# Kernel tuning notes

Hardware: AMD Instinct MI355X
Metric: run time of the kernel (lower is better)

## Reference

```python
import jax, jax.numpy as jnp
import numpy as np

N_NODES = 100000
N_EDGES = 1600000
IN_DIM = 128
OUT_DIM = 128
LEAKY_SLOPE = 0.01  # torch nn.LeakyReLU default


def setup_inputs() -> dict:
    key = jax.random.key(0)
    k1, k2, k3, k4 = jax.random.split(key, 4)
    x = jax.random.normal(k1, (N_NODES, IN_DIM), dtype=jnp.float32)
    edge_index = jax.random.randint(k2, (2, N_EDGES), 0, N_NODES, dtype=jnp.int64)
    edge_attr = jax.random.uniform(k3, (N_EDGES,), dtype=jnp.float32)
    # Linear params (xavier_uniform weight, zero bias)
    limit = np.sqrt(6.0 / (IN_DIM + OUT_DIM)).astype(np.float32)
    W = jax.random.uniform(k4, (OUT_DIM, IN_DIM), minval=-limit, maxval=limit, dtype=jnp.float32)
    b = jnp.zeros((OUT_DIM,), dtype=jnp.float32)
    return {"x": x, "edge_index": edge_index, "edge_attr": edge_attr, "W": W, "b": b}


def reference(x, edge_index, edge_attr, W, b):
    src = edge_index[0]  # x_j (source nodes)
    dst = edge_index[1]  # aggregation index (target nodes)
    # message: gather source features, scale by per-edge scalar  [E, D]
    msg = x[src] * edge_attr[:, None]
    # aggregate: scatter-add over target index  [N, D]
    agg = jax.ops.segment_sum(msg, dst, num_segments=N_NODES)
    # update: Linear + LeakyReLU (dropout is identity at p=0 / eval)
    out = agg @ W.T + b
    return jnp.where(out >= 0, out, LEAKY_SLOPE * out)
```

## Files before the change

kernel.cpp:

```cpp
#include <hip/hip_runtime.h>

#define N_NODES 100000
#define N_EDGES 1600000
#define DIM 128
#define LEAKY 0.01f
#define RS_STRIDE 132
#define WS_STRIDE 132
#define LSTRIDE 132
#define NBUCKET 391
#define SB_EDGES 4096
#define NSB 391

typedef short bf16x8 __attribute__((ext_vector_type(8)));
typedef float f32x4 __attribute__((ext_vector_type(4)));

static __device__ __forceinline__ unsigned short f2bf(float f) {
  unsigned int u = __float_as_uint(f);
  u = (u + 0x7fffu + ((u >> 16) & 1u)) >> 16;
  return (unsigned short)u;
}

__global__ __launch_bounds__(512) void sort_local_kernel(
    const int* __restrict__ ei, const float* __restrict__ attr,
    int2* __restrict__ binned, unsigned short* __restrict__ counts,
    int* __restrict__ srcOff) {
  __shared__ int hist[NBUCKET];
  __shared__ int cursor[NBUCKET];
  __shared__ int scanBuf[512];
  __shared__ int2 stage[SB_EDGES];

  const int t = threadIdx.x;
  const int blk = blockIdx.x;
  const int base = blk * SB_EDGES;
  const int n = min(SB_EDGES, N_EDGES - base);

  if (t < NBUCKET) hist[t] = 0;
  __syncthreads();

  int myP[8];
  int myB[8];
  float myA[8];
#pragma unroll
  for (int k = 0; k < 8; ++k) {
    int i = t + k * 512;
    if (i < n) {
      int e = base + i;
      int s = ei[e];
      int d = ei[N_EDGES + e];
      myA[k] = attr[e];
      myB[k] = d >> 8;
      myP[k] = s | ((d & 255) << 17);
      atomicAdd(&hist[myB[k]], 1);
    } else {
      myB[k] = -1;
    }
  }
  __syncthreads();

  int v = (t < NBUCKET) ? hist[t] : 0;
  scanBuf[t] = v;
  __syncthreads();
  for (int off = 1; off < 512; off <<= 1) {
    int u = (t >= off) ? scanBuf[t - off] : 0;
    __syncthreads();
    scanBuf[t] += u;
    __syncthreads();
  }
  if (t < NBUCKET) {
    int excl = scanBuf[t] - v;
    cursor[t] = excl;
    counts[(size_t)t * NSB + blk] = (unsigned short)v;
    srcOff[(size_t)t * NSB + blk] = base + excl;
  }
  __syncthreads();

#pragma unroll
  for (int k = 0; k < 8; ++k) {
    if (myB[k] >= 0) {
      int loc = atomicAdd(&cursor[myB[k]], 1);
      stage[loc] = make_int2(myP[k], __float_as_int(myA[k]));
    }
  }
  __syncthreads();

  for (int i = t; i < n; i += 512) binned[base + i] = stage[i];
}

__global__ __launch_bounds__(128) void bucket_count_kernel(
    const unsigned short* __restrict__ counts, int* __restrict__ bucketCount) {
  __shared__ int red[128];
  const int b = blockIdx.x;
  const int t = threadIdx.x;
  int s = 0;
  for (int sb = t; sb < NSB; sb += 128) s += counts[(size_t)b * NSB + sb];
  red[t] = s;
  __syncthreads();
  for (int off = 64; off > 0; off >>= 1) {
    if (t < off) red[t] += red[t + off];
    __syncthreads();
  }
  if (t == 0) bucketCount[b] = red[0];
}

__global__ __launch_bounds__(512) void bucket_scan_kernel(
    const int* __restrict__ bucketCount, int* __restrict__ bucketBase) {
  __shared__ int s[512];
  const int t = threadIdx.x;
  int v = (t < NBUCKET) ? bucketCount[t] : 0;
  s[t] = v;
  __syncthreads();
  for (int off = 1; off < 512; off <<= 1) {
    int u = (t >= off) ? s[t - off] : 0;
    __syncthreads();
    s[t] += u;
    __syncthreads();
  }
  if (t < NBUCKET) bucketBase[t] = s[t] - v;
}

__global__ __launch_bounds__(448) void passB_kernel(
    const int2* __restrict__ binned, const unsigned short* __restrict__ counts,
    const int* __restrict__ srcOff, const int* __restrict__ bucketBase,
    int2* __restrict__ csr, int* __restrict__ row_ptr) {
  __shared__ int runSrc[NSB];
  __shared__ int runLen[NSB];
  __shared__ int hist[256];
  __shared__ int cur[256];
  __shared__ int scanBuf[256];

  const int b = blockIdx.x;
  const int t = threadIdx.x;

  if (t < NSB) {
    runSrc[t] = srcOff[(size_t)b * NSB + t];
    runLen[t] = (int)counts[(size_t)b * NSB + t];
  }
  if (t < 256) hist[t] = 0;
  __syncthreads();

  if (t < NSB) {
    const int src = runSrc[t];
    const int len = runLen[t];
    for (int j = 0; j < len; ++j) {
      int px = binned[src + j].x;
      atomicAdd(&hist[(px >> 17) & 255], 1);
    }
  }
  __syncthreads();

  int hv = (t < 256) ? hist[t] : 0;
  if (t < 256) scanBuf[t] = hv;
  __syncthreads();
  for (int off = 1; off < 256; off <<= 1) {
    int u = 0;
    if (t < 256 && t >= off) u = scanBuf[t - off];
    __syncthreads();
    if (t < 256) scanBuf[t] += u;
    __syncthreads();
  }
  const int bb = bucketBase[b];
  if (t < 256) {
    int excl = scanBuf[t] - hv;
    cur[t] = excl;
    int node = b * 256 + t;
    if (node < N_NODES) row_ptr[node] = bb + excl;
  }
  if (b == 0 && t == 0) row_ptr[N_NODES] = N_EDGES;
  __syncthreads();

  if (t < NSB) {
    const int src = runSrc[t];
    const int len = runLen[t];
    for (int j = 0; j < len; ++j) {
      int2 rec = binned[src + j];
      int ld = (rec.x >> 17) & 255;
      int pos = bb + atomicAdd(&cur[ld], 1);
      csr[pos] = make_int2(rec.x & 0x1FFFF, rec.y);
    }
  }
}

__global__ __launch_bounds__(256) void x2b_kernel(
    const float4* __restrict__ x, ushort4* __restrict__ xb) {
  const int i = blockIdx.x * 256 + threadIdx.x;
  float4 v = x[i];
  ushort4 o;
  o.x = f2bf(v.x); o.y = f2bf(v.y); o.z = f2bf(v.z); o.w = f2bf(v.w);
  xb[i] = o;
}

__global__ __launch_bounds__(256) void gather_linear_kernel(
    const unsigned short* __restrict__ xb, const int* __restrict__ row_ptr,
    const int2* __restrict__ csr, const bf16x8* __restrict__ wfrag,
    const float* __restrict__ bias, float* __restrict__ out) {
  __shared__ float Ls[16 * LSTRIDE];

  const int w = threadIdx.x >> 6;
  const int lane = threadIdx.x & 63;
  const int nodeBase = blockIdx.x * 16;

#pragma unroll
  for (int k = 0; k < 4; ++k) {
    const int loc = w * 4 + k;
    const int node = nodeBase + loc;
    const int beg = row_ptr[node];
    const int end = row_ptr[node + 1];

    float2 acc = make_float2(0.f, 0.f);
    int e = beg;
    for (; e + 3 < end; e += 4) {
      int2 e0 = csr[e];
      int2 e1 = csr[e + 1];
      int2 e2 = csr[e + 2];
      int2 e3 = csr[e + 3];
      unsigned int u0 = *(const unsigned int*)(xb + (size_t)e0.x * DIM + lane * 2);
      unsigned int u1 = *(const unsigned int*)(xb + (size_t)e1.x * DIM + lane * 2);
      unsigned int u2 = *(const unsigned int*)(xb + (size_t)e2.x * DIM + lane * 2);
      unsigned int u3 = *(const unsigned int*)(xb + (size_t)e3.x * DIM + lane * 2);
      float a0 = __int_as_float(e0.y), a1 = __int_as_float(e1.y);
      float a2 = __int_as_float(e2.y), a3 = __int_as_float(e3.y);
      acc.x += __uint_as_float(u0 << 16) * a0;
      acc.y += __uint_as_float(u0 & 0xffff0000u) * a0;
      acc.x += __uint_as_float(u1 << 16) * a1;
      acc.y += __uint_as_float(u1 & 0xffff0000u) * a1;
      acc.x += __uint_as_float(u2 << 16) * a2;
      acc.y += __uint_as_float(u2 & 0xffff0000u) * a2;
      acc.x += __uint_as_float(u3 << 16) * a3;
      acc.y += __uint_as_float(u3 & 0xffff0000u) * a3;
    }
    for (; e < end; ++e) {
      int2 e0 = csr[e];
      float a0 = __int_as_float(e0.y);
      unsigned int u0 = *(const unsigned int*)(xb + (size_t)e0.x * DIM + lane * 2);
      acc.x += __uint_as_float(u0 << 16) * a0;
      acc.y += __uint_as_float(u0 & 0xffff0000u) * a0;
    }
    *(float2*)(Ls + loc * LSTRIDE + lane * 2) = acc;
  }
  __syncthreads();

  const int m = lane & 15;
  const int quad = lane >> 4;

  bf16x8 afrag[4];
#pragma unroll
  for (int q = 0; q < 4; ++q) {
    const float* ap = Ls + m * LSTRIDE + q * 32 + quad * 8;
    const float4 f0 = *(const float4*)(ap);
    const float4 f1 = *(const float4*)(ap + 4);
    afrag[q][0] = (short)f2bf(f0.x); afrag[q][1] = (short)f2bf(f0.y);
    afrag[q][2] = (short)f2bf(f0.z); afrag[q][3] = (short)f2bf(f0.w);
    afrag[q][4] = (short)f2bf(f1.x); afrag[q][5] = (short)f2bf(f1.y);
    afrag[q][6] = (short)f2bf(f1.z); afrag[q][7] = (short)f2bf(f1.w);
  }

#pragma unroll
  for (int j = 0; j < 2; ++j) {
    const int nt = w * 2 + j;
    const float bv = bias[nt * 16 + m];
    f32x4 acc = {bv, bv, bv, bv};
#pragma unroll
    for (int q = 0; q < 4; ++q) {
      bf16x8 bfrag = wfrag[(nt * 4 + q) * 64 + lane];
      acc = __builtin_amdgcn_mfma_f32_16x16x32_bf16(afrag[q], bfrag, acc, 0, 0, 0);
    }
    const int col = nt * 16 + m;
#pragma unroll
    for (int i = 0; i < 4; ++i) {
      float v = acc[i];
      v = v >= 0.f ? v : v * LEAKY;
      out[(size_t)(nodeBase + quad * 4 + i) * DIM + col] = v;
    }
  }
}

__global__ __launch_bounds__(256) void gather_f32_kernel(
    const float* __restrict__ x, const int* __restrict__ row_ptr,
    const int2* __restrict__ csr, float* __restrict__ out) {
  const int node = blockIdx.x * 4 + (threadIdx.x >> 6);
  const int lane = threadIdx.x & 63;

  const int beg = row_ptr[node];
  const int end = row_ptr[node + 1];

  float2 acc = make_float2(0.f, 0.f);
  int e = beg;
  for (; e + 3 < end; e += 4) {
    int2 e0 = csr[e];
    int2 e1 = csr[e + 1];
    int2 e2 = csr[e + 2];
    int2 e3 = csr[e + 3];
    float2 v0 = *(const float2*)(x + (size_t)e0.x * DIM + lane * 2);
    float2 v1 = *(const float2*)(x + (size_t)e1.x * DIM + lane * 2);
    float2 v2 = *(const float2*)(x + (size_t)e2.x * DIM + lane * 2);
    float2 v3 = *(const float2*)(x + (size_t)e3.x * DIM + lane * 2);
    float a0 = __int_as_float(e0.y), a1 = __int_as_float(e1.y);
    float a2 = __int_as_float(e2.y), a3 = __int_as_float(e3.y);
    acc.x += v0.x * a0; acc.y += v0.y * a0;
    acc.x += v1.x * a1; acc.y += v1.y * a1;
    acc.x += v2.x * a2; acc.y += v2.y * a2;
    acc.x += v3.x * a3; acc.y += v3.y * a3;
  }
  for (; e < end; ++e) {
    int2 e0 = csr[e];
    float a0 = __int_as_float(e0.y);
    float2 v0 = *(const float2*)(x + (size_t)e0.x * DIM + lane * 2);
    acc.x += v0.x * a0; acc.y += v0.y * a0;
  }
  *(float2*)(out + (size_t)node * DIM + lane * 2) = acc;
}

__global__ __launch_bounds__(256) void w_frag_kernel(
    const float* __restrict__ W, bf16x8* __restrict__ wfrag) {
  const int gid = blockIdx.x * 256 + threadIdx.x;
  const int lane = gid & 63;
  const int q = (gid >> 6) & 3;
  const int nt = gid >> 8;
  const int n = nt * 16 + (lane & 15);
  const int kb = q * 32 + ((lane >> 4) & 3) * 8;
  const float4 f0 = *(const float4*)(W + n * DIM + kb);
  const float4 f1 = *(const float4*)(W + n * DIM + kb + 4);
  bf16x8 frag;
  frag[0] = (short)f2bf(f0.x); frag[1] = (short)f2bf(f0.y);
  frag[2] = (short)f2bf(f0.z); frag[3] = (short)f2bf(f0.w);
  frag[4] = (short)f2bf(f1.x); frag[5] = (short)f2bf(f1.y);
  frag[6] = (short)f2bf(f1.z); frag[7] = (short)f2bf(f1.w);
  wfrag[gid] = frag;
}

__global__ __launch_bounds__(256) void linear_mfma_kernel(
    const float* __restrict__ agg, const bf16x8* __restrict__ wfrag,
    const float* __restrict__ bias, float* __restrict__ out) {
  const int wave = threadIdx.x >> 6;
  const int lane = threadIdx.x & 63;
  const int r0 = (blockIdx.x * 4 + wave) * 16;
  if (r0 >= N_NODES) return;

  const int m = lane & 15;
  const int quad = lane >> 4;
  const int row = r0 + m;

  bf16x8 afrag[4];
#pragma unroll
  for (int q = 0; q < 4; ++q) {
    const float* ap = agg + (size_t)row * DIM + q * 32 + quad * 8;
    const float4 f0 = *(const float4*)(ap);
    const float4 f1 = *(const float4*)(ap + 4);
    afrag[q][0] = (short)f2bf(f0.x); afrag[q][1] = (short)f2bf(f0.y);
    afrag[q][2] = (short)f2bf(f0.z); afrag[q][3] = (short)f2bf(f0.w);
    afrag[q][4] = (short)f2bf(f1.x); afrag[q][5] = (short)f2bf(f1.y);
    afrag[q][6] = (short)f2bf(f1.z); afrag[q][7] = (short)f2bf(f1.w);
  }

#pragma unroll
  for (int nt = 0; nt < 8; ++nt) {
    const float bv = bias[nt * 16 + m];
    f32x4 acc = {bv, bv, bv, bv};
#pragma unroll
    for (int q = 0; q < 4; ++q) {
      bf16x8 bfrag = wfrag[(nt * 4 + q) * 64 + lane];
      acc = __builtin_amdgcn_mfma_f32_16x16x32_bf16(afrag[q], bfrag, acc, 0, 0, 0);
    }
    const int col = nt * 16 + m;
#pragma unroll
    for (int i = 0; i < 4; ++i) {
      float v = acc[i];
      v = v >= 0.f ? v : v * LEAKY;
      out[(size_t)(r0 + quad * 4 + i) * DIM + col] = v;
    }
  }
}

__global__ __launch_bounds__(256) void scatter_kernel(
    const float* __restrict__ x, const int* __restrict__ ei,
    const float* __restrict__ attr, float* __restrict__ agg) {
  int gid = blockIdx.x * blockDim.x + threadIdx.x;
  int e = gid >> 5;
  int f = (gid & 31) * 4;
  if (e >= N_EDGES) return;
  int s = ei[e];
  int d = ei[N_EDGES + e];
  float a = attr[e];
  const float4 xv = *(const float4*)(x + (size_t)s * DIM + f);
  float* dp = agg + (size_t)d * DIM + f;
  atomicAdd(dp + 0, xv.x * a);
  atomicAdd(dp + 1, xv.y * a);
  atomicAdd(dp + 2, xv.z * a);
  atomicAdd(dp + 3, xv.w * a);
}

__global__ __launch_bounds__(256, 2) void linear_kernel(
    const float* __restrict__ agg, const float* __restrict__ W,
    const float* __restrict__ bias, float* __restrict__ out) {
  __shared__ float Rs[32 * RS_STRIDE];
  __shared__ float Ws[64 * WS_STRIDE];

  const int tid = threadIdx.x;
  const int c = (tid & 31) * 4;
  const int rg = tid >> 5;
  const size_t rowBase = (size_t)blockIdx.x * 32;

  {
    const int lr = tid >> 3;
    const int col = (tid & 7) * 16;
    const float4* src = (const float4*)(agg + (rowBase + lr) * DIM + col);
#pragma unroll
    for (int j = 0; j < 4; ++j) {
      *(float4*)(Rs + lr * RS_STRIDE + col + j * 4) = src[j];
    }
  }

  const float4 bv = *(const float4*)(bias + c);
  float4 acc0 = bv, acc1 = bv, acc2 = bv, acc3 = bv;

  for (int half = 0; half < 2; ++half) {
    __syncthreads();
    {
      const int k0 = tid >> 7;
      const int o = tid & 127;
#pragma unroll
      for (int kk = k0; kk < 64; kk += 2) {
        Ws[kk * WS_STRIDE + o] = W[o * DIM + half * 64 + kk];
      }
    }
    __syncthreads();

    const float* rs0 = Rs + (rg * 4 + 0) * RS_STRIDE + half * 64;
    const float* rs1 = Rs + (rg * 4 + 1) * RS_STRIDE + half * 64;
    const float* rs2 = Rs + (rg * 4 + 2) * RS_STRIDE + half * 64;
    const float* rs3 = Rs + (rg * 4 + 3) * RS_STRIDE + half * 64;

#pragma unroll 8
    for (int k4 = 0; k4 < 16; ++k4) {
      const float4 v0 = *(const float4*)(rs0 + k4 * 4);
      const float4 v1 = *(const float4*)(rs1 + k4 * 4);
      const float4 v2 = *(const float4*)(rs2 + k4 * 4);
      const float4 v3 = *(const float4*)(rs3 + k4 * 4);
      const float4 w0 = *(const float4*)(Ws + (k4 * 4 + 0) * WS_STRIDE + c);
      const float4 w1 = *(const float4*)(Ws + (k4 * 4 + 1) * WS_STRIDE + c);
      const float4 w2 = *(const float4*)(Ws + (k4 * 4 + 2) * WS_STRIDE + c);
      const float4 w3 = *(const float4*)(Ws + (k4 * 4 + 3) * WS_STRIDE + c);

#define FMA4(acc, v)                                               \
      acc.x += v.x * w0.x + v.y * w1.x + v.z * w2.x + v.w * w3.x;  \
      acc.y += v.x * w0.y + v.y * w1.y + v.z * w2.y + v.w * w3.y;  \
      acc.z += v.x * w0.z + v.y * w1.z + v.z * w2.z + v.w * w3.z;  \
      acc.w += v.x * w0.w + v.y * w1.w + v.z * w2.w + v.w * w3.w;
      FMA4(acc0, v0)
      FMA4(acc1, v1)
      FMA4(acc2, v2)
      FMA4(acc3, v3)
#undef FMA4
    }
  }

#define LEAKY4(acc)                                   \
  acc.x = acc.x >= 0.f ? acc.x : acc.x * LEAKY;       \
  acc.y = acc.y >= 0.f ? acc.y : acc.y * LEAKY;       \
  acc.z = acc.z >= 0.f ? acc.z : acc.z * LEAKY;       \
  acc.w = acc.w >= 0.f ? acc.w : acc.w * LEAKY;
  LEAKY4(acc0) LEAKY4(acc1) LEAKY4(acc2) LEAKY4(acc3)
#undef LEAKY4

  const int row0 = (int)rowBase + rg * 4;
  *(float4*)(out + (size_t)(row0 + 0) * DIM + c) = acc0;
  *(float4*)(out + (size_t)(row0 + 1) * DIM + c) = acc1;
  *(float4*)(out + (size_t)(row0 + 2) * DIM + c) = acc2;
  *(float4*)(out + (size_t)(row0 + 3) * DIM + c) = acc3;
}

extern "C" void kernel_launch(void* const* d_in, const int* in_sizes, int n_in,
                              void* d_out, int out_size, void* d_ws, size_t ws_size,
                              hipStream_t stream) {
  const float* x = (const float*)d_in[0];
  const int* ei = (const int*)d_in[1];
  const float* attr = (const float*)d_in[2];
  const float* W = (const float*)d_in[3];
  const float* b = (const float*)d_in[4];
  float* out = (float*)d_out;

  const size_t offBinned = 0;
  const size_t offCounts = 12812288;
  const size_t offSrcOff = offCounts + 305920;
  const size_t offBCount = offSrcOff + 611584;
  const size_t offBBase  = offBCount + 1792;
  const size_t offCsr    = offBBase + 1792;
  const size_t offRowPtr = offCsr + 12812288;
  const size_t offWfrag  = offRowPtr + 400128;
  const size_t sortNeed  = offWfrag + 32768;
  const size_t offXb     = sortNeed;
  const size_t fullNeed  = offXb + 25600000;

  if (ws_size >= sortNeed) {
    char* ws = (char*)d_ws;
    int2* binned = (int2*)(ws + offBinned);
    unsigned short* counts = (unsigned short*)(ws + offCounts);
    int* srcOff = (int*)(ws + offSrcOff);
    int* bucketCount = (int*)(ws + offBCount);
    int* bucketBase = (int*)(ws + offBBase);
    int2* csr = (int2*)(ws + offCsr);
    int* row_ptr = (int*)(ws + offRowPtr);
    bf16x8* wfrag = (bf16x8*)(ws + offWfrag);

    w_frag_kernel<<<8, 256, 0, stream>>>(W, wfrag);
    sort_local_kernel<<<NSB, 512, 0, stream>>>(ei, attr, binned, counts, srcOff);
    bucket_count_kernel<<<NBUCKET, 128, 0, stream>>>(counts, bucketCount);
    bucket_scan_kernel<<<1, 512, 0, stream>>>(bucketCount, bucketBase);
    passB_kernel<<<NBUCKET, 448, 0, stream>>>(binned, counts, srcOff, bucketBase,
                                              csr, row_ptr);
    if (ws_size >= fullNeed) {
      unsigned short* xb = (unsigned short*)(ws + offXb);
      x2b_kernel<<<12500, 256, 0, stream>>>((const float4*)x, (ushort4*)xb);
      gather_linear_kernel<<<N_NODES / 16, 256, 0, stream>>>(xb, row_ptr, csr,
                                                             wfrag, b, out);
    } else {
      gather_f32_kernel<<<N_NODES / 4, 256, 0, stream>>>(x, row_ptr, csr, out);
      linear_mfma_kernel<<<(N_NODES + 63) / 64, 256, 0, stream>>>(out, wfrag, b, out);
    }
  } else {
    hipMemsetAsync(out, 0, (size_t)N_NODES * DIM * sizeof(float), stream);
    scatter_kernel<<<(N_EDGES * 32) / 256, 256, 0, stream>>>(x, ei, attr, out);
    linear_kernel<<<N_NODES / 32, 256, 0, stream>>>(out, W, b, out);
  }
}
```

Measured before the change: 261.9 us.

## Split gather and linear, fuse x-to-bf16 conversion into sort kernel

Folds the fp32-to-bf16 conversion of x into the tail of the sort_local kernel, so the separate conversion launch disappears and the conversion runs alongside the sort. Replaces the fused gather+linear kernel with a one-node-per-wave gather that writes a bf16 aggregate buffer, followed by a separate MFMA linear kernel that loads bf16 fragments directly. This drops the LDS staging and barrier from the gather and raises its occupancy, at the cost of an extra 25.6 MB round trip through global memory for the aggregate and one more launch. It also needs more workspace, and falls back to the older paths when the workspace is too small.

```diff
diff --git a/kernel.cpp b/kernel.cpp
--- a/kernel.cpp
+++ b/kernel.cpp
@@ -6,7 +6,6 @@
 #define LEAKY 0.01f
 #define RS_STRIDE 132
 #define WS_STRIDE 132
-#define LSTRIDE 132
 #define NBUCKET 391
 #define SB_EDGES 4096
 #define NSB 391
@@ -23,7 +22,8 @@
 __global__ __launch_bounds__(512) void sort_local_kernel(
     const int* __restrict__ ei, const float* __restrict__ attr,
     int2* __restrict__ binned, unsigned short* __restrict__ counts,
-    int* __restrict__ srcOff) {
+    int* __restrict__ srcOff, const float4* __restrict__ x4,
+    ushort4* __restrict__ xb4) {
   __shared__ int hist[NBUCKET];
   __shared__ int cursor[NBUCKET];
   __shared__ int scanBuf[512];
@@ -84,6 +84,15 @@
   __syncthreads();
 
   for (int i = t; i < n; i += 512) binned[base + i] = stage[i];
+
+  if (xb4) {
+    for (int i = blk * 512 + t; i < (N_NODES * DIM) / 4; i += NSB * 512) {
+      float4 vv = x4[i];
+      ushort4 o;
+      o.x = f2bf(vv.x); o.y = f2bf(vv.y); o.z = f2bf(vv.z); o.w = f2bf(vv.w);
+      xb4[i] = o;
+    }
+  }
 }
 
 __global__ __launch_bounds__(128) void bucket_count_kernel(
@@ -180,98 +189,87 @@
   }
 }
 
-__global__ __launch_bounds__(256) void x2b_kernel(
-    const float4* __restrict__ x, ushort4* __restrict__ xb) {
-  const int i = blockIdx.x * 256 + threadIdx.x;
-  float4 v = x[i];
-  ushort4 o;
-  o.x = f2bf(v.x); o.y = f2bf(v.y); o.z = f2bf(v.z); o.w = f2bf(v.w);
-  xb[i] = o;
-}
-
-__global__ __launch_bounds__(256) void gather_linear_kernel(
+__global__ __launch_bounds__(256) void gather_aggb_kernel(
     const unsigned short* __restrict__ xb, const int* __restrict__ row_ptr,
-    const int2* __restrict__ csr, const bf16x8* __restrict__ wfrag,
-    const float* __restrict__ bias, float* __restrict__ out) {
-  __shared__ float Ls[16 * LSTRIDE];
-
-  const int w = threadIdx.x >> 6;
+    const int2* __restrict__ csr, unsigned int* __restrict__ aggB) {
+  const int node = blockIdx.x * 4 + (threadIdx.x >> 6);
   const int lane = threadIdx.x & 63;
-  const int nodeBase = blockIdx.x * 16;
-
-#pragma unroll
-  for (int k = 0; k < 4; ++k) {
-    const int loc = w * 4 + k;
-    const int node = nodeBase + loc;
-    const int beg = row_ptr[node];
-    const int end = row_ptr[node + 1];
-
-    float2 acc = make_float2(0.f, 0.f);
-    int e = beg;
-    for (; e + 3 < end; e += 4) {
-      int2 e0 = csr[e];
-      int2 e1 = csr[e + 1];
-      int2 e2 = csr[e + 2];
-      int2 e3 = csr[e + 3];
-      unsigned int u0 = *(const unsigned int*)(xb + (size_t)e0.x * DIM + lane * 2);
-      unsigned int u1 = *(const unsigned int*)(xb + (size_t)e1.x * DIM + lane * 2);
-      unsigned int u2 = *(const unsigned int*)(xb + (size_t)e2.x * DIM + lane * 2);
-      unsigned int u3 = *(const unsigned int*)(xb + (size_t)e3.x * DIM + lane * 2);
-      float a0 = __int_as_float(e0.y), a1 = __int_as_float(e1.y);
-      float a2 = __int_as_float(e2.y), a3 = __int_as_float(e3.y);
-      acc.x += __uint_as_float(u0 << 16) * a0;
-      acc.y += __uint_as_float(u0 & 0xffff0000u) * a0;
-      acc.x += __uint_as_float(u1 << 16) * a1;
-      acc.y += __uint_as_float(u1 & 0xffff0000u) * a1;
-      acc.x += __uint_as_float(u2 << 16) * a2;
-      acc.y += __uint_as_float(u2 & 0xffff0000u) * a2;
-      acc.x += __uint_as_float(u3 << 16) * a3;
-      acc.y += __uint_as_float(u3 & 0xffff0000u) * a3;
-    }
-    for (; e < end; ++e) {
-      int2 e0 = csr[e];
-      float a0 = __int_as_float(e0.y);
-      unsigned int u0 = *(const unsigned int*)(xb + (size_t)e0.x * DIM + lane * 2);
-      acc.x += __uint_as_float(u0 << 16) * a0;
-      acc.y += __uint_as_float(u0 & 0xffff0000u) * a0;
-    }
-    *(float2*)(Ls + loc * LSTRIDE + lane * 2) = acc;
-  }
-  __syncthreads();
-
-  const int m = lane & 15;
-  const int quad = lane >> 4;
-
-  bf16x8 afrag[4];
-#pragma unroll
-  for (int q = 0; q < 4; ++q) {
-    const float* ap = Ls + m * LSTRIDE + q * 32 + quad * 8;
-    const float4 f0 = *(const float4*)(ap);
-    const float4 f1 = *(const float4*)(ap + 4);
-    afrag[q][0] = (short)f2bf(f0.x); afrag[q][1] = (short)f2bf(f0.y);
-    afrag[q][2] = (short)f2bf(f0.z); afrag[q][3] = (short)f2bf(f0.w);
-    afrag[q][4] = (short)f2bf(f1.x); afrag[q][5] = (short)f2bf(f1.y);
-    afrag[q][6] = (short)f2bf(f1.z); afrag[q][7] = (short)f2bf(f1.w);
-  }
-
-#pragma unroll
-  for (int j = 0; j < 2; ++j) {
-    const int nt = w * 2 + j;
-    const float bv = bias[nt * 16 + m];
-    f32x4 acc = {bv, bv, bv, bv};
-#pragma unroll
-    for (int q = 0; q < 4; ++q) {
-      bf16x8 bfrag = wfrag[(nt * 4 + q) * 64 + lane];
-      acc = __builtin_amdgcn_mfma_f32_16x16x32_bf16(afrag[q], bfrag, acc, 0, 0, 0);
-    }
-    const int col = nt * 16 + m;
-#pragma unroll
-    for (int i = 0; i < 4; ++i) {
-      float v = acc[i];
-      v = v >= 0.f ? v : v * LEAKY;
-      out[(size_t)(nodeBase + quad * 4 + i) * DIM + col] = v;
-    }
-  }
+
+  const int beg = row_ptr[node];
+  const int end = row_ptr[node + 1];
+
+  float2 acc = make_float2(0.f, 0.f);
+  int e = beg;
+  for (; e + 3 < end; e += 4) {
+    int2 e0 = csr[e];
+    int2 e1 = csr[e + 1];
+    int2 e2 = csr[e + 2];
+    int2 e3 = csr[e + 3];
+    unsigned int u0 = *(const unsigned int*)(xb + (size_t)e0.x * DIM + lane * 2);
+    unsigned int u1 = *(const unsigned int*)(xb + (size_t)e1.x * DIM + lane * 2);
+    unsigned int u2 = *(const unsigned int*)(xb + (size_t)e2.x * DIM + lane * 2);
+    unsigned int u3 = *(const unsigned int*)(xb + (size_t)e3.x * DIM + lane * 2);
+    float a0 = __int_as_float(e0.y), a1 = __int_as_float(e1.y);
+    float a2 = __int_as_float(e2.y), a3 = __int_as_float(e3.y);
+    acc.x += __uint_as_float(u0 << 16) * a0;
+    acc.y += __uint_as_float(u0 & 0xffff0000u) * a0;
+    acc.x += __uint_as_float(u1 << 16) * a1;
+    acc.y += __uint_as_float(u1 & 0xffff0000u) * a1;
+    acc.x += __uint_as_float(u2 << 16) * a2;
+    acc.y += __uint_as_float(u2 & 0xffff0000u) * a2;
+    acc.x += __uint_as_float(u3 << 16) * a3;
+    acc.y += __uint_as_float(u3 & 0xffff0000u) * a3;
+  }
+  for (; e < end; ++e) {
+    int2 e0 = csr[e];
+    float a0 = __int_as_float(e0.y);
+    unsigned int u0 = *(const unsigned int*)(xb + (size_t)e0.x * DIM + lane * 2);
+    acc.x += __uint_as_float(u0 << 16) * a0;
+    acc.y += __uint_as_float(u0 & 0xffff0000u) * a0;
+  }
+  aggB[(size_t)node * 64 + lane] =
+      (unsigned int)f2bf(acc.x) | ((unsigned int)f2bf(acc.y) << 16);
+}
+
+__global__ __launch_bounds__(256) void gather_bf16_kernel(
+    const unsigned short* __restrict__ xb, const int* __restrict__ row_ptr,
+    const int2* __restrict__ csr, float* __restrict__ out) {
+  const int node = blockIdx.x * 4 + (threadIdx.x >> 6);
+  const int lane = threadIdx.x & 63;
+
+  const int beg = row_ptr[node];
+  const int end = row_ptr[node + 1];
+
+  float2 acc = make_float2(0.f, 0.f);
+  int e = beg;
+  for (; e + 3 < end; e += 4) {
+    int2 e0 = csr[e];
+    int2 e1 = csr[e + 1];
+    int2 e2 = csr[e + 2];
+    int2 e3 = csr[e + 3];
+    unsigned int u0 = *(const unsigned int*)(xb + (size_t)e0.x * DIM + lane * 2);
+    unsigned int u1 = *(const unsigned int*)(xb + (size_t)e1.x * DIM + lane * 2);
+    unsigned int u2 = *(const unsigned int*)(xb + (size_t)e2.x * DIM + lane * 2);
+    unsigned int u3 = *(const unsigned int*)(xb + (size_t)e3.x * DIM + lane * 2);
+    float a0 = __int_as_float(e0.y), a1 = __int_as_float(e1.y);
+    float a2 = __int_as_float(e2.y), a3 = __int_as_float(e3.y);
+    acc.x += __uint_as_float(u0 << 16) * a0;
+    acc.y += __uint_as_float(u0 & 0xffff0000u) * a0;
+    acc.x += __uint_as_float(u1 << 16) * a1;
+    acc.y += __uint_as_float(u1 & 0xffff0000u) * a1;
+    acc.x += __uint_as_float(u2 << 16) * a2;
+    acc.y += __uint_as_float(u2 & 0xffff0000u) * a2;
+    acc.x += __uint_as_float(u3 << 16) * a3;
+    acc.y += __uint_as_float(u3 & 0xffff0000u) * a3;
+  }
+  for (; e < end; ++e) {
+    int2 e0 = csr[e];
+    float a0 = __int_as_float(e0.y);
+    unsigned int u0 = *(const unsigned int*)(xb + (size_t)e0.x * DIM + lane * 2);
+    acc.x += __uint_as_float(u0 << 16) * a0;
+    acc.y += __uint_as_float(u0 & 0xffff0000u) * a0;
+  }
+  *(float2*)(out + (size_t)node * DIM + lane * 2) = acc;
 }
 
 __global__ __launch_bounds__(256) void gather_f32_kernel(
@@ -328,6 +326,43 @@
   wfrag[gid] = frag;
 }
 
+__global__ __launch_bounds__(256) void linear_mfma_bf16_kernel(
+    const unsigned short* __restrict__ aggB, const bf16x8* __restrict__ wfrag,
+    const float* __restrict__ bias, float* __restrict__ out) {
+  const int wave = threadIdx.x >> 6;
+  const int lane = threadIdx.x & 63;
+  const int r0 = (blockIdx.x * 4 + wave) * 16;
+  if (r0 >= N_NODES) return;
+
+  const int m = lane & 15;
+  const int quad = lane >> 4;
+  const int row = r0 + m;
+
+  bf16x8 afrag[4];
+#pragma unroll
+  for (int q = 0; q < 4; ++q) {
+    afrag[q] = *(const bf16x8*)(aggB + (size_t)row * DIM + q * 32 + quad * 8);
+  }
+
+#pragma unroll
+  for (int nt = 0; nt < 8; ++nt) {
+    const float bv = bias[nt * 16 + m];
+    f32x4 acc = {bv, bv, bv, bv};
+#pragma unroll
+    for (int q = 0; q < 4; ++q) {
+      bf16x8 bfrag = wfrag[(nt * 4 + q) * 64 + lane];
+      acc = __builtin_amdgcn_mfma_f32_16x16x32_bf16(afrag[q], bfrag, acc, 0, 0, 0);
+    }
+    const int col = nt * 16 + m;
+#pragma unroll
+    for (int i = 0; i < 4; ++i) {
+      float v = acc[i];
+      v = v >= 0.f ? v : v * LEAKY;
+      out[(size_t)(r0 + quad * 4 + i) * DIM + col] = v;
+    }
+  }
+}
+
 __global__ __launch_bounds__(256) void linear_mfma_kernel(
     const float* __restrict__ agg, const bf16x8* __restrict__ wfrag,
     const float* __restrict__ bias, float* __restrict__ out) {
@@ -369,6 +404,15 @@
       out[(size_t)(r0 + quad * 4 + i) * DIM + col] = v;
     }
   }
+}
+
+__global__ __launch_bounds__(256) void x2b_kernel(
+    const float4* __restrict__ x, ushort4* __restrict__ xb) {
+  const int i = blockIdx.x * 256 + threadIdx.x;
+  float4 v = x[i];
+  ushort4 o;
+  o.x = f2bf(v.x); o.y = f2bf(v.y); o.z = f2bf(v.z); o.w = f2bf(v.w);
+  xb[i] = o;
 }
 
 __global__ __launch_bounds__(256) void scatter_kernel(
@@ -490,6 +534,8 @@
   const size_t sortNeed  = offWfrag + 32768;
   const size_t offXb     = sortNeed;
   const size_t fullNeed  = offXb + 25600000;
+  const size_t offAggB   = fullNeed;
+  const size_t bf16Need  = offAggB + 25600000;
 
   if (ws_size >= sortNeed) {
     char* ws = (char*)d_ws;
@@ -501,18 +547,25 @@
     int2* csr = (int2*)(ws + offCsr);
     int* row_ptr = (int*)(ws + offRowPtr);
     bf16x8* wfrag = (bf16x8*)(ws + offWfrag);
+    const bool haveXb = ws_size >= fullNeed;
+    const bool haveAggB = ws_size >= bf16Need;
+    unsigned short* xb = haveXb ? (unsigned short*)(ws + offXb) : nullptr;
+    unsigned int* aggB = haveAggB ? (unsigned int*)(ws + offAggB) : nullptr;
 
     w_frag_kernel<<<8, 256, 0, stream>>>(W, wfrag);
-    sort_local_kernel<<<NSB, 512, 0, stream>>>(ei, attr, binned, counts, srcOff);
+    sort_local_kernel<<<NSB, 512, 0, stream>>>(ei, attr, binned, counts, srcOff,
+                                               (const float4*)x, (ushort4*)xb);
     bucket_count_kernel<<<NBUCKET, 128, 0, stream>>>(counts, bucketCount);
     bucket_scan_kernel<<<1, 512, 0, stream>>>(bucketCount, bucketBase);
     passB_kernel<<<NBUCKET, 448, 0, stream>>>(binned, counts, srcOff, bucketBase,
                                               csr, row_ptr);
-    if (ws_size >= fullNeed) {
-      unsigned short* xb = (unsigned short*)(ws + offXb);
-      x2b_kernel<<<12500, 256, 0, stream>>>((const float4*)x, (ushort4*)xb);
-      gather_linear_kernel<<<N_NODES / 16, 256, 0, stream>>>(xb, row_ptr, csr,
-                                                             wfrag, b, out);
+    if (haveAggB) {
+      gather_aggb_kernel<<<N_NODES / 4, 256, 0, stream>>>(xb, row_ptr, csr, aggB);
+      linear_mfma_bf16_kernel<<<(N_NODES + 63) / 64, 256, 0, stream>>>(
+          (const unsigned short*)aggB, wfrag, b, out);
+    } else if (haveXb) {
+      gather_bf16_kernel<<<N_NODES / 4, 256, 0, stream>>>(xb, row_ptr, csr, out);
+      linear_mfma_kernel<<<(N_NODES + 63) / 64, 256, 0, stream>>>(out, wfrag, b, out);
     } else {
       gather_f32_kernel<<<N_NODES / 4, 256, 0, stream>>>(x, row_ptr, csr, out);
       linear_mfma_kernel<<<(N_NODES + 63) / 64, 256, 0, stream>>>(out, wfrag, b, out);
```

Result: faster. 249.5 us (-4.7%).
